# Performance work log

Hardware: AMD Instinct MI355X
Metric: run time of the kernel (lower is better)

The kernel has to match this reference:

```python
import jax, jax.numpy as jnp
import numpy as np


def setup_inputs() -> dict:
    key = jax.random.key(0)
    X = jax.random.normal(key, (8, 64, 64, 64), dtype=jnp.float32)
    return {"X": X}


def reference(X):
    N, C, h, w = X.shape
    x1 = X.reshape(N, C, h * w)            # [N, C, HW]
    x2 = jnp.transpose(x1, (0, 2, 1))      # [N, HW, C]
    scores = jnp.einsum('bnc,bcm->bnm', x2, x1)  # [N, HW, HW]
    c = jax.nn.softmax(scores, axis=2)
    out = jnp.einsum('bnm,bmc->bnc', c, x2)      # [N, HW, C]
    out = jnp.transpose(out, (0, 2, 1)).reshape(N, C, h, w)
    return out
```

## Files before the change

### kernel.cpp

```cpp
#include <hip/hip_runtime.h>
#include <math.h>


#define SEQ 4096
#define DIM 64
#define LDB 72
#define LDO 68
#define LDO2 133
#define LDS2 68
#define QSCALE 1.2011224087864498f

typedef __attribute__((ext_vector_type(8)))  short short8;
typedef __attribute__((ext_vector_type(4)))  float f32x4;
typedef __attribute__((ext_vector_type(16))) float f32x16;

__device__ __forceinline__ unsigned short f2bf(float f) {
    union { float f; unsigned int u; } x; x.f = f;
    unsigned int u = x.u + 0x7FFFu + ((x.u >> 16) & 1u);
    return (unsigned short)(u >> 16);
}
__device__ __forceinline__ float bf2f(unsigned short h) {
    union { unsigned int u; float f; } x; x.u = ((unsigned int)h) << 16; return x.f;
}
__device__ __forceinline__ float fast_exp2(float x) {
#if __has_builtin(__builtin_amdgcn_exp2f)
    return __builtin_amdgcn_exp2f(x);
#else
    float r;
    asm("v_exp_f32 %0, %1\n\ts_nop 0" : "=v"(r) : "v"(x));
    return r;
#endif
}
__device__ __forceinline__ float fast_rcp(float x) {
#if __has_builtin(__builtin_amdgcn_rcpf)
    return __builtin_amdgcn_rcpf(x);
#else
    return 1.f / x;
#endif
}

__global__ __launch_bounds__(256) void prepass4(const float* __restrict__ X,
                                                unsigned short* __restrict__ Kf,
                                                unsigned short* __restrict__ Vf,
                                                float* __restrict__ Norms,
                                                float* __restrict__ MaxPart) {
    __shared__ __align__(16) unsigned short sT[64 * LDS2];
    __shared__ __align__(16) unsigned short sVu[64 * LDS2];
    __shared__ float sRed[4];
    const int b = blockIdx.y, m0 = blockIdx.x * 64;
    const float* Xb = X + (size_t)b * DIM * SEQ;
    const int t = threadIdx.x, w = t >> 6;
    const int mw = t & 15, cg = t >> 4;

    #pragma unroll
    for (int cr = 0; cr < 4; ++cr) {
        const int c = cg * 4 + cr;
        const f32x4 v = *(const f32x4*)(Xb + (size_t)c * SEQ + m0 + 4 * mw);
        *(ushort4*)(sVu + c * LDS2 + 4 * mw) =
            make_ushort4(f2bf(v.x), f2bf(v.y), f2bf(v.z), f2bf(v.w));
        sT[(4 * mw + 0) * LDS2 + c] = f2bf(v.x * QSCALE);
        sT[(4 * mw + 1) * LDS2 + c] = f2bf(v.y * QSCALE);
        sT[(4 * mw + 2) * LDS2 + c] = f2bf(v.z * QSCALE);
        sT[(4 * mw + 3) * LDS2 + c] = f2bf(v.w * QSCALE);
    }
    __syncthreads();

    {
        const int l = t & 63, ch = t >> 6;
        const int l31 = l & 31, hi = l >> 5;
        #pragma unroll
        for (int tl = 0; tl < 2; ++tl) {
            const short8 a = *(const short8*)(sT + (tl * 32 + l31) * LDS2 + ch * 16 + hi * 8);
            const size_t off = (size_t)b * 262144
                             + (size_t)(((m0 >> 5) + tl) * 4 + ch) * 512 + (size_t)l * 8;
            *(short8*)(Kf + off) = a;
        }
    }

    {
        const int m = t >> 2, ck = t & 3;
        const short8 a0 = *(const short8*)(sT + m * LDS2 + ck * 16);
        const short8 a1 = *(const short8*)(sT + m * LDS2 + ck * 16 + 8);
        float s = 0.f;
        #pragma unroll
        for (int i = 0; i < 8; ++i) {
            const float f0 = bf2f((unsigned short)a0[i]);
            const float f1 = bf2f((unsigned short)a1[i]);
            s += f0 * f0 + f1 * f1;
        }
        s += __shfl_xor(s, 1);
        s += __shfl_xor(s, 2);
        const float nm = sqrtf(s);
        if (ck == 0) Norms[(size_t)b * SEQ + m0 + m] = nm;

        float mx = nm;
        #pragma unroll
        for (int d = 4; d < 64; d <<= 1) mx = fmaxf(mx, __shfl_xor(mx, d));
        if ((t & 63) == 0) sRed[w] = mx;
    }

    {
        const int l = t & 63, pc = t >> 6;
        const int p = pc >> 1, ct = pc & 1;
        const int l31 = l & 31, hi = l >> 5;
        const int crow = (ct * 32 + l31) * LDS2;
        #pragma unroll
        for (int tl = 0; tl < 2; ++tl) {
            const int kbase = tl * 32 + p * 16 + hi * 4;
            const ushort4 g0 = *(const ushort4*)(sVu + crow + kbase);
            const ushort4 g1 = *(const ushort4*)(sVu + crow + kbase + 8);
            union { ushort4 g[2]; short8 v; } cat;
            cat.g[0] = g0; cat.g[1] = g1;
            const size_t off = (size_t)b * 262144
                             + (size_t)(((m0 >> 5) + tl) * 4 + p * 2 + ct) * 512 + (size_t)l * 8;
            *(short8*)(Vf + off) = cat.v;
        }
    }

    __syncthreads();
    if (t == 0)
        MaxPart[b * 64 + blockIdx.x] =
            fmaxf(fmaxf(sRed[0], sRed[1]), fmaxf(sRed[2], sRed[3]));
}

#if __has_builtin(__builtin_amdgcn_global_load_lds)
#define STAGE(BI, SOFF)                                                            \
    {                                                                              \
        unsigned short* dst_ = ring + (BI) * 4096 + (w ? 2048 : 0);                \
        const unsigned short* src_ = (w ? vgp : kgp) + (SOFF);                     \
        _Pragma("unroll")                                                          \
        for (int j_ = 0; j_ < 4; ++j_)                                             \
            __builtin_amdgcn_global_load_lds(                                      \
                (const __attribute__((address_space(1))) unsigned int*)(const void*)(src_ + j_ * 512), \
                (__attribute__((address_space(3))) unsigned int*)(void*)(dst_ + j_ * 512),             \
                16, 0, 0);                                                         \
    }
#else
#define STAGE(BI, SOFF)                                                            \
    {                                                                              \
        unsigned short* dst_ = ring + (BI) * 4096 + (w ? 2048 : 0) + lane * 8;     \
        const unsigned short* src_ = (w ? vgp : kgp) + (SOFF);                     \
        _Pragma("unroll")                                                          \
        for (int j_ = 0; j_ < 4; ++j_)                                             \
            *(short8*)(dst_ + j_ * 512) = *(const short8*)(src_ + j_ * 512);       \
    }
#endif

#define ATTN_STEP32(KF, VF)                                                        \
    {                                                                              \
        f32x16 aq0 = cin16[0], aq1 = cin16[1];                                     \
        _Pragma("unroll")                                                          \
        for (int ch_ = 0; ch_ < 4; ++ch_)                                          \
            aq0 = __builtin_amdgcn_mfma_f32_32x32x16_bf16(KF[ch_], qf[0][ch_], aq0, 0, 0, 0); \
        _Pragma("unroll")                                                          \
        for (int ch_ = 0; ch_ < 4; ++ch_)                                          \
            aq1 = __builtin_amdgcn_mfma_f32_32x32x16_bf16(KF[ch_], qf[1][ch_], aq1, 0, 0, 0); \
        short8 pa_[2][2];                                                          \
        _Pragma("unroll")                                                          \
        for (int qt_ = 0; qt_ < 2; ++qt_) {                                        \
            const f32x16 aa_ = qt_ ? aq1 : aq0;                                    \
            float p_[16];                                                          \
            _Pragma("unroll")                                                      \
            for (int r_ = 0; r_ < 16; ++r_) p_[r_] = fast_exp2(aa_[r_]);           \
            lp4[qt_] += (f32x4){p_[0], p_[1], p_[2], p_[3]};                       \
            lp4[qt_] += (f32x4){p_[4], p_[5], p_[6], p_[7]};                       \
            lp4[qt_] += (f32x4){p_[8], p_[9], p_[10], p_[11]};                     \
            lp4[qt_] += (f32x4){p_[12], p_[13], p_[14], p_[15]};                   \
            _Pragma("unroll")                                                      \
            for (int ph_ = 0; ph_ < 2; ++ph_) {                                    \
                union { unsigned u[4]; short8 v; } pk_;                            \
                _Pragma("unroll")                                                  \
                for (int k_ = 0; k_ < 4; ++k_)                                     \
                    pk_.u[k_] = __builtin_amdgcn_perm(                             \
                        __float_as_uint(p_[8 * ph_ + 2 * k_ + 1]),                 \
                        __float_as_uint(p_[8 * ph_ + 2 * k_]), 0x07060302u);       \
                pa_[qt_][ph_] = pk_.v;                                             \
            }                                                                      \
        }                                                                          \
        _Pragma("unroll")                                                          \
        for (int qt_ = 0; qt_ < 2; ++qt_) {                                        \
            _Pragma("unroll")                                                      \
            for (int ct_ = 0; ct_ < 2; ++ct_) {                                    \
                acc_o[qt_][ct_] = __builtin_amdgcn_mfma_f32_32x32x16_bf16(         \
                    pa_[qt_][0], VF[0][ct_], acc_o[qt_][ct_], 0, 0, 0);            \
                acc_o[qt_][ct_] = __builtin_amdgcn_mfma_f32_32x32x16_bf16(         \
                    pa_[qt_][1], VF[1][ct_], acc_o[qt_][ct_], 0, 0, 0);            \
            }                                                                      \
        }                                                                          \
    }

template <bool PARTIAL>
__global__ __launch_bounds__(128, 2) void attn_split4(const unsigned short* __restrict__ Kf,
                                                      const unsigned short* __restrict__ Vf,
                                                      const float* __restrict__ Norms,
                                                      const float* __restrict__ MaxPart,
                                                      unsigned short* __restrict__ Obf,
                                                      float* __restrict__ Lbase,
                                                      float* __restrict__ Out,
                                                      int niter) {
    __shared__ __align__(16) unsigned char smem[34048];
    unsigned short* ring = (unsigned short*)smem;
    float*          sO   = (float*)smem;

    const int tid  = threadIdx.x;
    const int lane = tid & 63;
    const int w    = tid >> 6;
    const int l31  = lane & 31;
    const int hi   = lane >> 5;

    const int gid  = blockIdx.x + 32 * (blockIdx.y + 8 * blockIdx.z);
    const int b    = gid & 7;
    const int rest = gid >> 3;
    const int s0   = (rest & 31) * 128;
    const int h    = rest >> 5;
    const int kt0  = h * niter;
    const unsigned short* Kfb = Kf + (size_t)b * 262144;
    const unsigned short* Vfb = Vf + (size_t)b * 262144;

    float mxn = MaxPart[b * 64 + lane];
    #pragma unroll
    for (int d = 1; d < 64; d <<= 1) mxn = fmaxf(mxn, __shfl_xor(mxn, d));

    short8 qf[2][4];
    f32x16 cin16[2];
    const int qtile = (s0 + 64 * w) >> 5;
    #pragma unroll
    for (int qt = 0; qt < 2; ++qt) {
        #pragma unroll
        for (int ch = 0; ch < 4; ++ch)
            qf[qt][ch] = *(const short8*)(Kfb
                + (size_t)((qtile + qt) * 4 + ch) * 512 + lane * 8);
        const float mrow = Norms[(size_t)b * SEQ + s0 + 64 * w + 32 * qt + l31] * mxn;
        #pragma unroll
        for (int r = 0; r < 16; ++r) cin16[qt][r] = -mrow;
    }

    f32x16 acc_o[2][2];
    #pragma unroll
    for (int qt = 0; qt < 2; ++qt)
        #pragma unroll
        for (int ct = 0; ct < 2; ++ct)
            #pragma unroll
            for (int r = 0; r < 16; ++r) acc_o[qt][ct][r] = 0.f;
    f32x4 lp4[2];
    lp4[0] = (f32x4){0.f, 0.f, 0.f, 0.f};
    lp4[1] = (f32x4){0.f, 0.f, 0.f, 0.f};

    const unsigned short* kgp = Kfb + lane * 8;
    const unsigned short* vgp = Vfb + lane * 8;

    STAGE(0, (size_t)kt0 * 2048);
    __syncthreads();

    for (int it = 0; it < niter; ++it) {
        const int cur = it & 1;
        if (it + 1 < niter)
            STAGE(cur ^ 1, (size_t)(kt0 + it + 1) * 2048);

        const unsigned short* Kb = ring + cur * 4096;
        const unsigned short* Vb = Kb + 2048;
        short8 kf[4], vf[2][2];
        #pragma unroll
        for (int ch = 0; ch < 4; ++ch)
            kf[ch] = *(const short8*)(Kb + ch * 512 + lane * 8);
        #pragma unroll
        for (int p = 0; p < 2; ++p)
            #pragma unroll
            for (int ct = 0; ct < 2; ++ct)
                vf[p][ct] = *(const short8*)(Vb + (p * 2 + ct) * 512 + lane * 8);

        ATTN_STEP32(kf, vf);
        __syncthreads();
    }

    float lp[2];
    #pragma unroll
    for (int qt = 0; qt < 2; ++qt) {
        lp[qt] = (lp4[qt][0] + lp4[qt][1]) + (lp4[qt][2] + lp4[qt][3]);
        lp[qt] += __shfl_xor(lp[qt], 32);
    }

    if (PARTIAL) {
        if (hi == 0) {
            #pragma unroll
            for (int qt = 0; qt < 2; ++qt)
                (Lbase + (size_t)h * 8 * SEQ)[(size_t)b * SEQ + s0 + 64 * w + 32 * qt + l31] = lp[qt];
        }
    } else {
        #pragma unroll
        for (int qt = 0; qt < 2; ++qt) {
            #pragma unroll
            for (int r = 0; r < 16; ++r) {
                const float inv = fast_rcp(__shfl(lp[qt], (r & 3) + 8 * (r >> 2) + 4 * hi));
                #pragma unroll
                for (int ct = 0; ct < 2; ++ct) acc_o[qt][ct][r] *= inv;
            }
        }
    }

    __syncthreads();
    #pragma unroll
    for (int qt = 0; qt < 2; ++qt)
        #pragma unroll
        for (int ct = 0; ct < 2; ++ct) {
            const int c = ct * 32 + l31;
            #pragma unroll
            for (int r = 0; r < 16; ++r)
                sO[c * LDO2 + 64 * w + 32 * qt + (r & 3) + 8 * (r >> 2) + 4 * hi] = acc_o[qt][ct][r];
        }
    __syncthreads();
    const int mw = tid & 31, cg = tid >> 5;
    if (PARTIAL) {
        unsigned short* Op = Obf + (size_t)h * 8 * DIM * SEQ;
        #pragma unroll
        for (int cc = 0; cc < 16; ++cc) {
            const int c = cg + 4 * cc;
            const f32x4 v = *(const f32x4*)(sO + c * LDO2 + 4 * mw);
            *(ushort4*)(Op + ((size_t)b * DIM + c) * SEQ + s0 + 4 * mw) =
                make_ushort4(f2bf(v.x), f2bf(v.y), f2bf(v.z), f2bf(v.w));
        }
    } else {
        #pragma unroll
        for (int cc = 0; cc < 16; ++cc) {
            const int c = cg + 4 * cc;
            const f32x4 v = *(const f32x4*)(sO + c * LDO2 + 4 * mw);
            *(f32x4*)(Out + ((size_t)b * DIM + c) * SEQ + s0 + 4 * mw) = v;
        }
    }
}

__global__ __launch_bounds__(256) void combine4(const unsigned short* __restrict__ Obf,
                                                const float* __restrict__ Lp,
                                                float* __restrict__ Out) {
    const int gid = blockIdx.x * 256 + threadIdx.x;
    const size_t base = (size_t)gid * 4;
    const int s = (int)(base & 4095);
    const int b = (int)(base >> 18);
    f32x4 os = (f32x4){0.f, 0.f, 0.f, 0.f};
    f32x4 ls = (f32x4){0.f, 0.f, 0.f, 0.f};
    #pragma unroll
    for (int h = 0; h < 4; ++h) {
        const ushort4 o = *(const ushort4*)(Obf + (size_t)h * 2097152 + base);
        os[0] += bf2f(o.x); os[1] += bf2f(o.y); os[2] += bf2f(o.z); os[3] += bf2f(o.w);
        const f32x4 l = *(const f32x4*)(Lp + (size_t)h * 8 * SEQ + b * SEQ + s);
        #pragma unroll
        for (int i = 0; i < 4; ++i) ls[i] += l[i];
    }
    f32x4 o;
    #pragma unroll
    for (int i = 0; i < 4; ++i) o[i] = os[i] / ls[i];
    *(f32x4*)(Out + base) = o;
}

__global__ __launch_bounds__(256, 2) void attn_fallback(const float* __restrict__ X,
                                                        float* __restrict__ Out) {
    __shared__ __align__(16) unsigned char smem[27648];
    unsigned short* sK = (unsigned short*)smem;
    unsigned short* sV = (unsigned short*)(smem + 9216);
    unsigned short* sP = (unsigned short*)(smem + 18432);
    float*          sO = (float*)smem;
    const int tid  = threadIdx.x;
    const int lane = tid & 63;
    const int w    = tid >> 6;
    const int l15  = lane & 15;
    const int quad = lane >> 4;
    const int b  = blockIdx.y;
    const int s0 = blockIdx.x * 64;
    const float* Xb = X + (size_t)b * DIM * SEQ;
    const int mgrp = tid & 15;
    const int c0   = tid >> 4;

    for (int cc = 0; cc < 4; ++cc) {
        int c = c0 + 16 * cc;
        const f32x4 v = *(const f32x4*)(Xb + (size_t)c * SEQ + s0 + 4 * mgrp);
        sK[(4 * mgrp + 0) * LDB + c] = f2bf(v.x);
        sK[(4 * mgrp + 1) * LDB + c] = f2bf(v.y);
        sK[(4 * mgrp + 2) * LDB + c] = f2bf(v.z);
        sK[(4 * mgrp + 3) * LDB + c] = f2bf(v.w);
    }
    __syncthreads();
    short8 qf0, qf1;
    {
        const int row = 16 * w + l15;
        qf0 = *(const short8*)(sK + row * LDB + quad * 8);
        qf1 = *(const short8*)(sK + row * LDB + 32 + quad * 8);
    }
    __syncthreads();
    f32x4 acc_o[4];
    for (int ct = 0; ct < 4; ++ct) acc_o[ct] = (f32x4){0.f, 0.f, 0.f, 0.f};
    float m_i[4] = {-1e30f, -1e30f, -1e30f, -1e30f};
    float l_i[4] = {0.f, 0.f, 0.f, 0.f};
    for (int kt = 0; kt < SEQ / 64; ++kt) {
        const int m0 = kt * 64;
        for (int cc = 0; cc < 4; ++cc) {
            int c = c0 + 16 * cc;
            const f32x4 v = *(const f32x4*)(Xb + (size_t)c * SEQ + m0 + 4 * mgrp);
            unsigned short h0 = f2bf(v.x), h1 = f2bf(v.y), h2 = f2bf(v.z), h3 = f2bf(v.w);
            *(ushort4*)(sV + c * LDB + 4 * mgrp) = make_ushort4(h0, h1, h2, h3);
            sK[(4 * mgrp + 0) * LDB + c] = h0;
            sK[(4 * mgrp + 1) * LDB + c] = h1;
            sK[(4 * mgrp + 2) * LDB + c] = h2;
            sK[(4 * mgrp + 3) * LDB + c] = h3;
        }
        __syncthreads();
        short8 vf[2][4];
        for (int ks = 0; ks < 2; ++ks)
            for (int ct = 0; ct < 4; ++ct)
                vf[ks][ct] = *(const short8*)(sV + (16 * ct + l15) * LDB + ks * 32 + quad * 8);
        f32x4 acc_s[4];
        for (int mt = 0; mt < 4; ++mt) {
            const int row = 16 * mt + l15;
            const short8 kf0 = *(const short8*)(sK + row * LDB + quad * 8);
            const short8 kf1 = *(const short8*)(sK + row * LDB + 32 + quad * 8);
            f32x4 a = (f32x4){0.f, 0.f, 0.f, 0.f};
            a = __builtin_amdgcn_mfma_f32_16x16x32_bf16(qf0, kf0, a, 0, 0, 0);
            a = __builtin_amdgcn_mfma_f32_16x16x32_bf16(qf1, kf1, a, 0, 0, 0);
            acc_s[mt] = a;
        }
        float alpha[4];
        for (int r = 0; r < 4; ++r) {
            float mx = fmaxf(fmaxf(acc_s[0][r], acc_s[1][r]), fmaxf(acc_s[2][r], acc_s[3][r]));
            mx = fmaxf(mx, __shfl_xor(mx, 1));
            mx = fmaxf(mx, __shfl_xor(mx, 2));
            mx = fmaxf(mx, __shfl_xor(mx, 4));
            mx = fmaxf(mx, __shfl_xor(mx, 8));
            const float mnew = fmaxf(m_i[r], mx);
            alpha[r] = __expf(m_i[r] - mnew);
            m_i[r] = mnew;
        }
        float rowsum[4] = {0.f, 0.f, 0.f, 0.f};
        unsigned short pb[4][4];
        for (int mt = 0; mt < 4; ++mt)
            for (int r = 0; r < 4; ++r) {
                const float p = __expf(acc_s[mt][r] - m_i[r]);
                rowsum[r] += p;
                pb[mt][r] = f2bf(p);
            }
        for (int r = 0; r < 4; ++r) {
            float s = rowsum[r];
            s += __shfl_xor(s, 1);
            s += __shfl_xor(s, 2);
            s += __shfl_xor(s, 4);
            s += __shfl_xor(s, 8);
            l_i[r] = alpha[r] * l_i[r] + s;
        }
        for (int ct = 0; ct < 4; ++ct)
            for (int r = 0; r < 4; ++r)
                acc_o[ct][r] *= alpha[r];
        for (int mt = 0; mt < 4; ++mt)
            for (int r = 0; r < 4; ++r)
                sP[(16 * w + quad * 4 + r) * LDB + l15 + 16 * mt] = pb[mt][r];
        __syncthreads();
        const short8 pf0 = *(const short8*)(sP + (16 * w + l15) * LDB + quad * 8);
        const short8 pf1 = *(const short8*)(sP + (16 * w + l15) * LDB + 32 + quad * 8);
        for (int ct = 0; ct < 4; ++ct) {
            acc_o[ct] = __builtin_amdgcn_mfma_f32_16x16x32_bf16(pf0, vf[0][ct], acc_o[ct], 0, 0, 0);
            acc_o[ct] = __builtin_amdgcn_mfma_f32_16x16x32_bf16(pf1, vf[1][ct], acc_o[ct], 0, 0, 0);
        }
    }
    float inv[4];
    for (int r = 0; r < 4; ++r) inv[r] = 1.f / l_i[r];
    for (int ct = 0; ct < 4; ++ct) {
        const int c = 16 * ct + l15;
        for (int r = 0; r < 4; ++r)
            sO[c * LDO + 16 * w + quad * 4 + r] = acc_o[ct][r] * inv[r];
    }
    __syncthreads();
    for (int cc = 0; cc < 4; ++cc) {
        const int c = c0 + 16 * cc;
        const f32x4 v = *(const f32x4*)(sO + c * LDO + 4 * mgrp);
        *(f32x4*)(Out + (size_t)b * DIM * SEQ + (size_t)c * SEQ + s0 + 4 * mgrp) = v;
    }
}

extern "C" void kernel_launch(void* const* d_in, const int* in_sizes, int n_in,
                              void* d_out, int out_size, void* d_ws, size_t ws_size,
                              hipStream_t stream) {
    const float* X = (const float*)d_in[0];
    float* Out = (float*)d_out;
    const size_t elems = (size_t)8 * SEQ * DIM;
    const size_t offVf    = elems * 2;
    const size_t offNorms = offVf + elems * 2;
    const size_t offMaxP  = offNorms + (size_t)8 * SEQ * 4;
    const size_t offObf   = offMaxP + 8 * 64 * 4;
    const size_t offLp    = offObf + 4 * elems * 2;
    const size_t need     = offLp + 4 * (size_t)8 * SEQ * 4;

    if (ws_size >= need) {
        unsigned short* Kf = (unsigned short*)d_ws;
        unsigned short* Vf = (unsigned short*)((char*)d_ws + offVf);
        float* Norms   = (float*)((char*)d_ws + offNorms);
        float* MaxPart = (float*)((char*)d_ws + offMaxP);
        unsigned short* Obf = (unsigned short*)((char*)d_ws + offObf);
        float* Lp = (float*)((char*)d_ws + offLp);
        prepass4<<<dim3(64, 8), 256, 0, stream>>>(X, Kf, Vf, Norms, MaxPart);
        attn_split4<true><<<dim3(32, 8, 4), 128, 0, stream>>>(Kf, Vf, Norms, MaxPart,
                                                              Obf, Lp, nullptr, 32);
        combine4<<<(int)(elems / 1024), 256, 0, stream>>>(Obf, Lp, Out);
    } else {
        attn_fallback<<<dim3(64, 8), 256, 0, stream>>>(X, Out);
    }
}
```

Measured before the change: 109.0 us.

## Halve per-warp query tile to one 32-row MFMA tile, doubling block count

Each wave now processes a single 32-query tile instead of two, so a block covers 64 queries and the grid doubles to 64x8x4 blocks. The accumulator and register footprint halves, shared memory drops to 17 KB, and launch bounds rise to 4 blocks per CU to improve occupancy. In exchange, each K/V tile staged into LDS is reused by half as many queries, which doubles the K/V load traffic per unit of compute.

```diff
diff --git a/kernel.cpp b/kernel.cpp
--- a/kernel.cpp
+++ b/kernel.cpp
@@ -6,7 +6,6 @@
 #define DIM 64
 #define LDB 72
 #define LDO 68
-#define LDO2 133
 #define LDS2 68
 #define QSCALE 1.2011224087864498f
 
@@ -148,49 +147,39 @@
 
 #define ATTN_STEP32(KF, VF)                                                        \
     {                                                                              \
-        f32x16 aq0 = cin16[0], aq1 = cin16[1];                                     \
+        f32x16 aq = cin16;                                                         \
         _Pragma("unroll")                                                          \
         for (int ch_ = 0; ch_ < 4; ++ch_)                                          \
-            aq0 = __builtin_amdgcn_mfma_f32_32x32x16_bf16(KF[ch_], qf[0][ch_], aq0, 0, 0, 0); \
-        _Pragma("unroll")                                                          \
-        for (int ch_ = 0; ch_ < 4; ++ch_)                                          \
-            aq1 = __builtin_amdgcn_mfma_f32_32x32x16_bf16(KF[ch_], qf[1][ch_], aq1, 0, 0, 0); \
-        short8 pa_[2][2];                                                          \
-        _Pragma("unroll")                                                          \
-        for (int qt_ = 0; qt_ < 2; ++qt_) {                                        \
-            const f32x16 aa_ = qt_ ? aq1 : aq0;                                    \
-            float p_[16];                                                          \
+            aq = __builtin_amdgcn_mfma_f32_32x32x16_bf16(KF[ch_], qf[ch_], aq, 0, 0, 0); \
+        float p_[16];                                                              \
+        _Pragma("unroll")                                                          \
+        for (int r_ = 0; r_ < 16; ++r_) p_[r_] = fast_exp2(aq[r_]);                \
+        lp4 += (f32x4){p_[0], p_[1], p_[2], p_[3]};                                \
+        lp4 += (f32x4){p_[4], p_[5], p_[6], p_[7]};                                \
+        lp4 += (f32x4){p_[8], p_[9], p_[10], p_[11]};                              \
+        lp4 += (f32x4){p_[12], p_[13], p_[14], p_[15]};                            \
+        short8 pa_[2];                                                             \
+        _Pragma("unroll")                                                          \
+        for (int ph_ = 0; ph_ < 2; ++ph_) {                                        \
+            union { unsigned u[4]; short8 v; } pk_;                                \
             _Pragma("unroll")                                                      \
-            for (int r_ = 0; r_ < 16; ++r_) p_[r_] = fast_exp2(aa_[r_]);           \
-            lp4[qt_] += (f32x4){p_[0], p_[1], p_[2], p_[3]};                       \
-            lp4[qt_] += (f32x4){p_[4], p_[5], p_[6], p_[7]};                       \
-            lp4[qt_] += (f32x4){p_[8], p_[9], p_[10], p_[11]};                     \
-            lp4[qt_] += (f32x4){p_[12], p_[13], p_[14], p_[15]};                   \
-            _Pragma("unroll")                                                      \
-            for (int ph_ = 0; ph_ < 2; ++ph_) {                                    \
-                union { unsigned u[4]; short8 v; } pk_;                            \
-                _Pragma("unroll")                                                  \
-                for (int k_ = 0; k_ < 4; ++k_)                                     \
-                    pk_.u[k_] = __builtin_amdgcn_perm(                             \
-                        __float_as_uint(p_[8 * ph_ + 2 * k_ + 1]),                 \
-                        __float_as_uint(p_[8 * ph_ + 2 * k_]), 0x07060302u);       \
-                pa_[qt_][ph_] = pk_.v;                                             \
-            }                                                                      \
+            for (int k_ = 0; k_ < 4; ++k_)                                         \
+                pk_.u[k_] = __builtin_amdgcn_perm(                                 \
+                    __float_as_uint(p_[8 * ph_ + 2 * k_ + 1]),                     \
+                    __float_as_uint(p_[8 * ph_ + 2 * k_]), 0x07060302u);           \
+            pa_[ph_] = pk_.v;                                                      \
         }                                                                          \
         _Pragma("unroll")                                                          \
-        for (int qt_ = 0; qt_ < 2; ++qt_) {                                        \
-            _Pragma("unroll")                                                      \
-            for (int ct_ = 0; ct_ < 2; ++ct_) {                                    \
-                acc_o[qt_][ct_] = __builtin_amdgcn_mfma_f32_32x32x16_bf16(         \
-                    pa_[qt_][0], VF[0][ct_], acc_o[qt_][ct_], 0, 0, 0);            \
-                acc_o[qt_][ct_] = __builtin_amdgcn_mfma_f32_32x32x16_bf16(         \
-                    pa_[qt_][1], VF[1][ct_], acc_o[qt_][ct_], 0, 0, 0);            \
-            }                                                                      \
+        for (int ct_ = 0; ct_ < 2; ++ct_) {                                        \
+            acc_o[ct_] = __builtin_amdgcn_mfma_f32_32x32x16_bf16(                  \
+                pa_[0], VF[0][ct_], acc_o[ct_], 0, 0, 0);                          \
+            acc_o[ct_] = __builtin_amdgcn_mfma_f32_32x32x16_bf16(                  \
+                pa_[1], VF[1][ct_], acc_o[ct_], 0, 0, 0);                          \
         }                                                                          \
     }
 
 template <bool PARTIAL>
-__global__ __launch_bounds__(128, 2) void attn_split4(const unsigned short* __restrict__ Kf,
+__global__ __launch_bounds__(128, 4) void attn_split4(const unsigned short* __restrict__ Kf,
                                                       const unsigned short* __restrict__ Vf,
                                                       const float* __restrict__ Norms,
                                                       const float* __restrict__ MaxPart,
@@ -198,7 +187,7 @@
                                                       float* __restrict__ Lbase,
                                                       float* __restrict__ Out,
                                                       int niter) {
-    __shared__ __align__(16) unsigned char smem[34048];
+    __shared__ __align__(16) unsigned char smem[17408];
     unsigned short* ring = (unsigned short*)smem;
     float*          sO   = (float*)smem;
 
@@ -208,11 +197,11 @@
     const int l31  = lane & 31;
     const int hi   = lane >> 5;
 
-    const int gid  = blockIdx.x + 32 * (blockIdx.y + 8 * blockIdx.z);
+    const int gid  = blockIdx.x + 64 * (blockIdx.y + 8 * blockIdx.z);
     const int b    = gid & 7;
     const int rest = gid >> 3;
-    const int s0   = (rest & 31) * 128;
-    const int h    = rest >> 5;
+    const int s0   = (rest & 63) * 64;
+    const int h    = rest >> 6;
     const int kt0  = h * niter;
     const unsigned short* Kfb = Kf + (size_t)b * 262144;
     const unsigned short* Vfb = Vf + (size_t)b * 262144;
@@ -221,30 +210,24 @@
     #pragma unroll
     for (int d = 1; d < 64; d <<= 1) mxn = fmaxf(mxn, __shfl_xor(mxn, d));
 
-    short8 qf[2][4];
-    f32x16 cin16[2];
-    const int qtile = (s0 + 64 * w) >> 5;
-    #pragma unroll
-    for (int qt = 0; qt < 2; ++qt) {
-        #pragma unroll
-        for (int ch = 0; ch < 4; ++ch)
-            qf[qt][ch] = *(const short8*)(Kfb
-                + (size_t)((qtile + qt) * 4 + ch) * 512 + lane * 8);
-        const float mrow = Norms[(size_t)b * SEQ + s0 + 64 * w + 32 * qt + l31] * mxn;
-        #pragma unroll
-        for (int r = 0; r < 16; ++r) cin16[qt][r] = -mrow;
-    }
-
-    f32x16 acc_o[2][2];
-    #pragma unroll
-    for (int qt = 0; qt < 2; ++qt)
-        #pragma unroll
-        for (int ct = 0; ct < 2; ++ct)
-            #pragma unroll
-            for (int r = 0; r < 16; ++r) acc_o[qt][ct][r] = 0.f;
-    f32x4 lp4[2];
-    lp4[0] = (f32x4){0.f, 0.f, 0.f, 0.f};
-    lp4[1] = (f32x4){0.f, 0.f, 0.f, 0.f};
+    short8 qf[4];
+    const int qtile = (s0 >> 5) + w;
+    #pragma unroll
+    for (int ch = 0; ch < 4; ++ch)
+        qf[ch] = *(const short8*)(Kfb + (size_t)(qtile * 4 + ch) * 512 + lane * 8);
+    f32x16 cin16;
+    {
+        const float mrow = Norms[(size_t)b * SEQ + s0 + 32 * w + l31] * mxn;
+        #pragma unroll
+        for (int r = 0; r < 16; ++r) cin16[r] = -mrow;
+    }
+
+    f32x16 acc_o[2];
+    #pragma unroll
+    for (int ct = 0; ct < 2; ++ct)
+        #pragma unroll
+        for (int r = 0; r < 16; ++r) acc_o[ct][r] = 0.f;
+    f32x4 lp4 = (f32x4){0.f, 0.f, 0.f, 0.f};
 
     const unsigned short* kgp = Kfb + lane * 8;
     const unsigned short* vgp = Vfb + lane * 8;
@@ -273,57 +256,45 @@
         __syncthreads();
     }
 
-    float lp[2];
-    #pragma unroll
-    for (int qt = 0; qt < 2; ++qt) {
-        lp[qt] = (lp4[qt][0] + lp4[qt][1]) + (lp4[qt][2] + lp4[qt][3]);
-        lp[qt] += __shfl_xor(lp[qt], 32);
-    }
+    float lp = (lp4[0] + lp4[1]) + (lp4[2] + lp4[3]);
+    lp += __shfl_xor(lp, 32);
 
     if (PARTIAL) {
-        if (hi == 0) {
+        if (hi == 0)
+            (Lbase + (size_t)h * 8 * SEQ)[(size_t)b * SEQ + s0 + 32 * w + l31] = lp;
+    } else {
+        #pragma unroll
+        for (int r = 0; r < 16; ++r) {
+            const float inv = fast_rcp(__shfl(lp, (r & 3) + 8 * (r >> 2) + 4 * hi));
             #pragma unroll
-            for (int qt = 0; qt < 2; ++qt)
-                (Lbase + (size_t)h * 8 * SEQ)[(size_t)b * SEQ + s0 + 64 * w + 32 * qt + l31] = lp[qt];
-        }
-    } else {
-        #pragma unroll
-        for (int qt = 0; qt < 2; ++qt) {
-            #pragma unroll
-            for (int r = 0; r < 16; ++r) {
-                const float inv = fast_rcp(__shfl(lp[qt], (r & 3) + 8 * (r >> 2) + 4 * hi));
-                #pragma unroll
-                for (int ct = 0; ct < 2; ++ct) acc_o[qt][ct][r] *= inv;
-            }
-        }
-    }
-
-    __syncthreads();
-    #pragma unroll
-    for (int qt = 0; qt < 2; ++qt)
-        #pragma unroll
-        for (int ct = 0; ct < 2; ++ct) {
-            const int c = ct * 32 + l31;
-            #pragma unroll
-            for (int r = 0; r < 16; ++r)
-                sO[c * LDO2 + 64 * w + 32 * qt + (r & 3) + 8 * (r >> 2) + 4 * hi] = acc_o[qt][ct][r];
-        }
-    __syncthreads();
-    const int mw = tid & 31, cg = tid >> 5;
+            for (int ct = 0; ct < 2; ++ct) acc_o[ct][r] *= inv;
+        }
+    }
+
+    __syncthreads();
+    #pragma unroll
+    for (int ct = 0; ct < 2; ++ct) {
+        const int c = ct * 32 + l31;
+        #pragma unroll
+        for (int r = 0; r < 16; ++r)
+            sO[c * LDO + 32 * w + (r & 3) + 8 * (r >> 2) + 4 * hi] = acc_o[ct][r];
+    }
+    __syncthreads();
+    const int mw = tid & 15, cg = tid >> 4;
     if (PARTIAL) {
         unsigned short* Op = Obf + (size_t)h * 8 * DIM * SEQ;
         #pragma unroll
-        for (int cc = 0; cc < 16; ++cc) {
-            const int c = cg + 4 * cc;
-            const f32x4 v = *(const f32x4*)(sO + c * LDO2 + 4 * mw);
+        for (int cc = 0; cc < 8; ++cc) {
+            const int c = cg + 8 * cc;
+            const f32x4 v = *(const f32x4*)(sO + c * LDO + 4 * mw);
             *(ushort4*)(Op + ((size_t)b * DIM + c) * SEQ + s0 + 4 * mw) =
                 make_ushort4(f2bf(v.x), f2bf(v.y), f2bf(v.z), f2bf(v.w));
         }
     } else {
         #pragma unroll
-        for (int cc = 0; cc < 16; ++cc) {
-            const int c = cg + 4 * cc;
-            const f32x4 v = *(const f32x4*)(sO + c * LDO2 + 4 * mw);
+        for (int cc = 0; cc < 8; ++cc) {
+            const int c = cg + 8 * cc;
+            const f32x4 v = *(const f32x4*)(sO + c * LDO + 4 * mw);
             *(f32x4*)(Out + ((size_t)b * DIM + c) * SEQ + s0 + 4 * mw) = v;
         }
     }
@@ -494,7 +465,7 @@
         unsigned short* Obf = (unsigned short*)((char*)d_ws + offObf);
         float* Lp = (float*)((char*)d_ws + offLp);
         prepass4<<<dim3(64, 8), 256, 0, stream>>>(X, Kf, Vf, Norms, MaxPart);
-        attn_split4<true><<<dim3(32, 8, 4), 128, 0, stream>>>(Kf, Vf, Norms, MaxPart,
+        attn_split4<true><<<dim3(64, 8, 4), 128, 0, stream>>>(Kf, Vf, Norms, MaxPart,
                                                               Obf, Lp, nullptr, 32);
         combine4<<<(int)(elems / 1024), 256, 0, stream>>>(Obf, Lp, Out);
     } else {
```

Result: no change. 110.5 us (+1.3%).
